# Performance work log

Hardware: AMD Instinct MI355X
Metric: run time of the kernel (lower is better)

Reference implementation:

```python
import jax, jax.numpy as jnp
import numpy as np

HF8_BIAS = 14  # exponent bias for the 1-4-3 hf8 layout; HF8_MAX = 2^(15-14)*1.875 = 3.75


def hf8_decode(bits):
    """Decode 8-bit hf8 codes (1 sign, 4 exp, 3 mantissa) to float.

    Mirrors convert.hf8_to_fp16: an elementwise dequant producing the
    fp16-valued weight tensor (computed here in fp32 for reference accuracy).
    """
    bits = bits.astype(jnp.int32)
    sign = jnp.where(((bits >> 7) & 1) == 1, -1.0, 1.0)
    exp = (bits >> 3) & 0xF
    man = (bits & 0x7).astype(jnp.float32)
    normal = jnp.exp2((exp - HF8_BIAS).astype(jnp.float32)) * (1.0 + man / 8.0)
    subnormal = jnp.exp2(jnp.float32(1 - HF8_BIAS)) * (man / 8.0)
    return sign * jnp.where(exp == 0, subnormal, normal)


def setup_inputs() -> dict:
    key = jax.random.key(0)
    k1, k2, k3 = jax.random.split(key, 3)
    B, Cin, Cout, H, W, K = 8, 320, 320, 64, 64, 3
    x = jax.random.normal(k1, (B, Cin, H, W), dtype=jnp.float32)
    w_bits = jax.random.randint(k2, (Cout, Cin, K, K), 0, 256, dtype=jnp.int32)
    b_bits = jax.random.randint(k3, (Cout,), 0, 256, dtype=jnp.int32)
    return {"x": x, "w_bits": w_bits, "b_bits": b_bits}


def reference(x, w_bits, b_bits):
    # dequant hf8 -> dense weight/bias (the fusible elementwise pass)
    w = hf8_decode(w_bits)          # [Cout, Cin, K, K]
    b = hf8_decode(b_bits)          # [Cout]
    # padding_mode == 'zeros' branch: plain conv2d, stride 1, pad 1, dilation 1, groups 1
    out = jax.lax.conv_general_dilated(
        x, w,
        window_strides=(1, 1),
        padding=((1, 1), (1, 1)),
        rhs_dilation=(1, 1),
        dimension_numbers=("NCHW", "OIHW", "NCHW"),
        feature_group_count=1,
    )
    return out + b[None, :, None, None]
```

## Files before the change

kernel.cpp:

```cpp
#include <hip/hip_runtime.h>
#include <stdint.h>

typedef short v8s __attribute__((ext_vector_type(8)));
typedef float v4f __attribute__((ext_vector_type(4)));
typedef unsigned int u32;

#define CIN   320
#define COUT  320
#define HH    64
#define WW    64
#define BN    80
#define NT    10
#define XSB   25344
#define WLB   15360
#define WKHB  61440

__device__ __forceinline__ float hf8_decode_f(int b) {
    int e = (b >> 3) & 15;
    int m = b & 7;
    float v = ldexpf((float)(e ? (8 + m) : m), e ? (e - 17) : -16);
    return ((b >> 7) & 1) ? -v : v;
}

__device__ __forceinline__ u32 cvt_pk_bf16(float lo, float hi) {
    u32 r;
    asm("v_cvt_pk_bf16_f32 %0, %1, %2" : "=v"(r) : "v"(lo), "v"(hi));
    return r;
}

__device__ __forceinline__ void gload16(const void* g, void* l) {
    __builtin_amdgcn_global_load_lds(
        (const __attribute__((address_space(1))) u32*)(uintptr_t)g,
        (__attribute__((address_space(3))) u32*)(uintptr_t)l, 16, 0, 0);
}

__global__ __launch_bounds__(256) void prepass_kernel(const int* __restrict__ w_bits,
                                                      const int* __restrict__ b_bits,
                                                      const float* __restrict__ x,
                                                      unsigned short* __restrict__ w_deq2,
                                                      float* __restrict__ b_deq,
                                                      unsigned short* __restrict__ x_t) {
    __shared__ __align__(16) unsigned short lt[32 * 64];
    const int tid = threadIdx.x;
    if (blockIdx.x < 3600) {
        int o  = blockIdx.x * 256 + tid;
        int e  = o & 7;
        int c2 = o >> 3;
        int co = c2 % COUT;
        int c3 = c2 / COUT;
        int cig = c3 & 3;
        int c4 = c3 >> 2;
        int kw = c4 % 3;
        int c5 = c4 / 3;
        int kh = c5 % 3;
        int t  = c5 / 3;
        int ci = t * 32 + cig * 8 + e;
        float v = hf8_decode_f(w_bits[(co * CIN + ci) * 9 + kh * 3 + kw] & 0xFF);
        w_deq2[o] = (unsigned short)(__float_as_uint(v) >> 16);
        if (o < COUT) b_deq[o] = hf8_decode_f(b_bits[o] & 0xFF);
        return;
    }
    const int b  = blockIdx.x - 3600;
    const int hp = b % 66;
    const int nc = b / 66;
    char* outp = (char*)x_t + (size_t)b * 4096;
    if (hp == 0 || hp == 65) {
        *(int4*)(outp + tid * 16) = make_int4(0, 0, 0, 0);
        return;
    }
    const int h = hp - 1;
    {
        int ci = tid >> 3, wg = tid & 7;
        const float* src = x + ((size_t)nc * 32 + ci) * (HH * WW) + h * WW + wg * 8;
        float4 a = *(const float4*)src;
        float4 c = *(const float4*)(src + 4);
        u32 d0 = cvt_pk_bf16(a.x, a.y);
        u32 d1 = cvt_pk_bf16(a.z, a.w);
        u32 d2 = cvt_pk_bf16(c.x, c.y);
        u32 d3 = cvt_pk_bf16(c.z, c.w);
        *(int4*)&lt[ci * 64 + wg * 8] = make_int4(d0, d1, d2, d3);
    }
    __syncthreads();
    if (tid < 128) {
        int w2 = tid & 31, o = tid >> 5;
        u32 A[4], B[4];
        #pragma unroll
        for (int j = 0; j < 4; ++j) {
            int p = o * 4 + j;
            u32 de = *(const u32*)&lt[(2 * p) * 64 + w2 * 2];
            u32 dq = *(const u32*)&lt[(2 * p + 1) * 64 + w2 * 2];
            A[j] = __builtin_amdgcn_perm(dq, de, 0x05040100u);
            B[j] = __builtin_amdgcn_perm(dq, de, 0x07060302u);
        }
        *(int4*)(outp + (2 * w2) * 64 + o * 16)     = make_int4(A[0], A[1], A[2], A[3]);
        *(int4*)(outp + (2 * w2 + 1) * 64 + o * 16) = make_int4(B[0], B[1], B[2], B[3]);
    }
}

__global__ __launch_bounds__(128, 1) void conv_phase_kernel(
        const unsigned short* __restrict__ x_t,
        const unsigned short* __restrict__ w_deq2,
        const float* __restrict__ b_deq,
        float* __restrict__ out) {
    __shared__ __align__(16) unsigned short xs[2 * XSB / 2];
    __shared__ __align__(16) unsigned short wl[2 * WLB / 2];

    const int tid  = threadIdx.x;
    const int bid  = blockIdx.x;
    const int cob  = bid >> 7;
    const int mb   = bid & 127;
    const int n    = mb >> 4;
    const int h0   = (mb & 15) << 2;
    const int wave = tid >> 6;
    const int lane = tid & 63;
    const int lhi  = lane >> 4;
    const int llo  = lane & 15;

    for (int i = tid; i < 384; i += 128) {
        int buf = i / 192;
        int r   = (i - buf * 192) >> 5;
        int rem = i & 31;
        int side = rem >> 4, e = rem & 15;
        *(u32*)((char*)xs + buf * XSB + r * 4224 + side * 4160 + e * 4) = 0;
    }

    int woffW[8];
    #pragma unroll
    for (int k = 0; k < 8; ++k) {
        int c = k * 128 + tid;
        int q = c / BN;
        int co = c - q * BN;
        woffW[k] = (q * COUT + cob * BN + co) << 4;
    }

    v4f acc[2][4][5];
    #pragma unroll
    for (int r = 0; r < 2; ++r)
        #pragma unroll
        for (int wc = 0; wc < 4; ++wc)
            #pragma unroll
            for (int j = 0; j < 5; ++j)
                acc[r][wc][j] = (v4f){0.f, 0.f, 0.f, 0.f};

    const char* xt_base = (const char*)x_t + ((size_t)(n * NT) * 66 + h0) * 4096;

    auto issueW = [&](int t_, int kh_, int wb) {
        const char* base = (const char*)w_deq2 + (size_t)(t_ * 3 + kh_) * WKHB;
        char* dst = (char*)wl + wb * WLB + tid * 16;
        #pragma unroll
        for (int k = 0; k < 8; ++k) {
            if (k * 128 + tid < 960)
                gload16(base + woffW[k], dst + k * 2048);
        }
    };
    auto issueX = [&](int t_, int xb) {
        const char* src = xt_base + (size_t)t_ * (66 * 4096);
        char* dstb = (char*)xs + xb * XSB;
        #pragma unroll
        for (int k = 0; k < 12; ++k) {
            int c = k * 128 + tid;
            int j = c >> 8;
            int u = c & 255;
            gload16(src + j * 4096 + u * 16, dstb + j * 4224 + 64 + u * 16);
        }
    };
    auto computeKh = [&](int kh, int xb, int wb) {
        const char* xp = (const char*)xs + xb * XSB + (2 * wave + kh) * 4224;
        const unsigned short* wp = wl + wb * (WLB / 2);
        __builtin_amdgcn_s_setprio(1);
        #pragma unroll
        for (int kw = 0; kw < 3; ++kw) {
            v8s bfr[5];
            #pragma unroll
            for (int nr = 0; nr < 5; ++nr)
                bfr[nr] = *(const v8s*)&wp[((kw * 4 + lhi) * BN + nr * 16 + llo) * 8];
            #pragma unroll
            for (int r = 0; r < 2; ++r)
                #pragma unroll
                for (int wc = 0; wc < 4; ++wc) {
                    v8s afr = *(const v8s*)(xp + r * 4224 + (wc * 16 + llo + kw) * 64 + lhi * 16);
                    #pragma unroll
                    for (int nr = 0; nr < 5; ++nr)
                        acc[r][wc][nr] = __builtin_amdgcn_mfma_f32_16x16x32_bf16(
                            afr, bfr[nr], acc[r][wc][nr], 0, 0, 0);
                }
        }
        __builtin_amdgcn_s_setprio(0);
    };

    issueW(0, 0, 0);
    issueX(0, 0);

    for (int t = 0; t < NT; ++t) {
        const int p = t & 1;
        __syncthreads();
        issueW(t, 1, p ^ 1);
        computeKh(0, p, p);
        __syncthreads();
        issueW(t, 2, p);
        computeKh(1, p, p ^ 1);
        __syncthreads();
        if (t + 1 < NT) { issueW(t + 1, 0, p ^ 1); issueX(t + 1, p ^ 1); }
        computeKh(2, p, p);
    }

    #pragma unroll
    for (int nr = 0; nr < 5; ++nr) {
        int co = cob * BN + nr * 16 + llo;
        float bias = b_deq[co];
        #pragma unroll
        for (int r = 0; r < 2; ++r) {
            int h = h0 + 2 * wave + r;
            float* op = out + ((size_t)(n * COUT + co) * HH + h) * WW + lhi * 4;
            #pragma unroll
            for (int wc = 0; wc < 4; ++wc) {
                float4 o;
                o.x = acc[r][wc][nr][0] + bias;
                o.y = acc[r][wc][nr][1] + bias;
                o.z = acc[r][wc][nr][2] + bias;
                o.w = acc[r][wc][nr][3] + bias;
                *(float4*)(op + wc * 16) = o;
            }
        }
    }
}

extern "C" void kernel_launch(void* const* d_in, const int* in_sizes, int n_in,
                              void* d_out, int out_size, void* d_ws, size_t ws_size,
                              hipStream_t stream) {
    const float* x      = (const float*)d_in[0];
    const int*   w_bits = (const int*)d_in[1];
    const int*   b_bits = (const int*)d_in[2];
    float*       out    = (float*)d_out;

    unsigned short* w_deq2 = (unsigned short*)d_ws;
    float*          b_deq  = (float*)((char*)d_ws + 1843200);
    unsigned short* x_t    = (unsigned short*)((char*)d_ws + (2u << 20));

    prepass_kernel<<<8880, 256, 0, stream>>>(w_bits, b_bits, x, w_deq2, b_deq, x_t);
    conv_phase_kernel<<<512, 128, 0, stream>>>(x_t, w_deq2, b_deq, out);
}
```

Baseline: 74.19 us.

## Restructure conv into 4-wave blocks with per-tap triple-buffered weight pipeline

The conv kernel moves from 2 waves with 2 output rows each to 4 waves with one row each, and asks for 2 blocks per CU. Weights are now streamed one (kh,kw) tap at a time into a triple-buffered LDS ring. Loads are issued two taps ahead, with explicit vmcnt waits and one barrier per tap instead of full-kh double buffering. The aim is to raise occupancy, shrink LDS per block, and overlap global-to-LDS loads with MFMA work more finely, at the cost of more barriers and hand-tuned waitcnt counts that must match the number of outstanding loads.

```diff
diff --git a/kernel.cpp b/kernel.cpp
--- a/kernel.cpp
+++ b/kernel.cpp
@@ -5,15 +5,15 @@
 typedef float v4f __attribute__((ext_vector_type(4)));
 typedef unsigned int u32;
 
-#define CIN   320
-#define COUT  320
-#define HH    64
-#define WW    64
-#define BN    80
-#define NT    10
-#define XSB   25344
-#define WLB   15360
-#define WKHB  61440
+#define CIN    320
+#define COUT   320
+#define HH     64
+#define WW     64
+#define BN     80
+#define NT     10
+#define XSB    25344
+#define WLBUF  5120
+#define WSLICE 20480
 
 __device__ __forceinline__ float hf8_decode_f(int b) {
     int e = (b >> 3) & 15;
@@ -37,7 +37,7 @@
 __global__ __launch_bounds__(256) void prepass_kernel(const int* __restrict__ w_bits,
                                                       const int* __restrict__ b_bits,
                                                       const float* __restrict__ x,
-                                                      unsigned short* __restrict__ w_deq2,
+                                                      unsigned short* __restrict__ w_deq3,
                                                       float* __restrict__ b_deq,
                                                       unsigned short* __restrict__ x_t) {
     __shared__ __align__(16) unsigned short lt[32 * 64];
@@ -49,14 +49,13 @@
         int co = c2 % COUT;
         int c3 = c2 / COUT;
         int cig = c3 & 3;
-        int c4 = c3 >> 2;
-        int kw = c4 % 3;
-        int c5 = c4 / 3;
-        int kh = c5 % 3;
-        int t  = c5 / 3;
+        int g  = c3 >> 2;
+        int kw = g % 3;
+        int kh = (g / 3) % 3;
+        int t  = g / 9;
         int ci = t * 32 + cig * 8 + e;
         float v = hf8_decode_f(w_bits[(co * CIN + ci) * 9 + kh * 3 + kw] & 0xFF);
-        w_deq2[o] = (unsigned short)(__float_as_uint(v) >> 16);
+        w_deq3[o] = (unsigned short)(__float_as_uint(v) >> 16);
         if (o < COUT) b_deq[o] = hf8_decode_f(b_bits[o] & 0xFF);
         return;
     }
@@ -97,13 +96,13 @@
     }
 }
 
-__global__ __launch_bounds__(128, 1) void conv_phase_kernel(
+__global__ __launch_bounds__(256, 2) void conv_t4_kernel(
         const unsigned short* __restrict__ x_t,
-        const unsigned short* __restrict__ w_deq2,
+        const unsigned short* __restrict__ w_deq3,
         const float* __restrict__ b_deq,
         float* __restrict__ out) {
     __shared__ __align__(16) unsigned short xs[2 * XSB / 2];
-    __shared__ __align__(16) unsigned short wl[2 * WLB / 2];
+    __shared__ __align__(16) unsigned short wl[3 * WLBUF / 2];
 
     const int tid  = threadIdx.x;
     const int bid  = blockIdx.x;
@@ -116,7 +115,7 @@
     const int lhi  = lane >> 4;
     const int llo  = lane & 15;
 
-    for (int i = tid; i < 384; i += 128) {
+    for (int i = tid; i < 384; i += 256) {
         int buf = i / 192;
         int r   = (i - buf * 192) >> 5;
         int rem = i & 31;
@@ -124,103 +123,105 @@
         *(u32*)((char*)xs + buf * XSB + r * 4224 + side * 4160 + e * 4) = 0;
     }
 
-    int woffW[8];
-    #pragma unroll
-    for (int k = 0; k < 8; ++k) {
-        int c = k * 128 + tid;
-        int q = c / BN;
-        int co = c - q * BN;
-        woffW[k] = (q * COUT + cob * BN + co) << 4;
-    }
-
-    v4f acc[2][4][5];
-    #pragma unroll
-    for (int r = 0; r < 2; ++r)
-        #pragma unroll
-        for (int wc = 0; wc < 4; ++wc)
-            #pragma unroll
-            for (int j = 0; j < 5; ++j)
-                acc[r][wc][j] = (v4f){0.f, 0.f, 0.f, 0.f};
-
-    const char* xt_base = (const char*)x_t + ((size_t)(n * NT) * 66 + h0) * 4096;
-
-    auto issueW = [&](int t_, int kh_, int wb) {
-        const char* base = (const char*)w_deq2 + (size_t)(t_ * 3 + kh_) * WKHB;
-        char* dst = (char*)wl + wb * WLB + tid * 16;
-        #pragma unroll
-        for (int k = 0; k < 8; ++k) {
-            if (k * 128 + tid < 960)
-                gload16(base + woffW[k], dst + k * 2048);
-        }
+    int woffW[2], wdst[2];
+    #pragma unroll
+    for (int k = 0; k < 2; ++k) {
+        int jj  = wave * 2 + k;
+        int cmb = (jj * 64) % 320;
+        int cm  = cmb + lane;
+        int cig = cm / BN;
+        int co  = cm - cig * BN;
+        woffW[k] = (cig * COUT + cob * BN + co) << 4;
+        wdst[k]  = cmb << 4;
+    }
+
+    v4f acc[4][5];
+    #pragma unroll
+    for (int i = 0; i < 4; ++i)
+        #pragma unroll
+        for (int j = 0; j < 5; ++j)
+            acc[i][j] = (v4f){0.f, 0.f, 0.f, 0.f};
+
+    const char* xt_lane = (const char*)x_t + ((size_t)(n * NT) * 66 + h0) * 4096 + lane * 16;
+
+    auto issueW = [&](int g, int buf) {
+        const char* base = (const char*)w_deq3 + (size_t)g * WSLICE;
+        char* dst = (char*)wl + buf * WLBUF;
+        gload16(base + woffW[0], dst + wdst[0]);
+        gload16(base + woffW[1], dst + wdst[1]);
     };
-    auto issueX = [&](int t_, int xb) {
-        const char* src = xt_base + (size_t)t_ * (66 * 4096);
-        char* dstb = (char*)xs + xb * XSB;
-        #pragma unroll
-        for (int k = 0; k < 12; ++k) {
-            int c = k * 128 + tid;
-            int j = c >> 8;
-            int u = c & 255;
-            gload16(src + j * 4096 + u * 16, dstb + j * 4224 + 64 + u * 16);
-        }
+    auto issueX1 = [&](int tt, int xb, int m) {
+        int id = wave * 6 + m;
+        int j = id >> 2, k = id & 3;
+        gload16(xt_lane + (size_t)tt * (66 * 4096) + j * 4096 + k * 1024,
+                (char*)xs + xb * XSB + j * 4224 + 64 + k * 1024);
     };
-    auto computeKh = [&](int kh, int xb, int wb) {
-        const char* xp = (const char*)xs + xb * XSB + (2 * wave + kh) * 4224;
-        const unsigned short* wp = wl + wb * (WLB / 2);
+    auto phaseCompute = [&](int kh, int kw, int xb, int buf) {
+        const unsigned short* wp = (const unsigned short*)((const char*)wl + buf * WLBUF);
+        const char* xp = (const char*)xs + xb * XSB + (wave + kh) * 4224;
+        v8s bfr[5];
+        #pragma unroll
+        for (int nr = 0; nr < 5; ++nr)
+            bfr[nr] = *(const v8s*)&wp[(lhi * BN + nr * 16 + llo) * 8];
         __builtin_amdgcn_s_setprio(1);
         #pragma unroll
-        for (int kw = 0; kw < 3; ++kw) {
-            v8s bfr[5];
+        for (int mr = 0; mr < 4; ++mr) {
+            v8s afr = *(const v8s*)(xp + (mr * 16 + llo + kw) * 64 + lhi * 16);
             #pragma unroll
             for (int nr = 0; nr < 5; ++nr)
-                bfr[nr] = *(const v8s*)&wp[((kw * 4 + lhi) * BN + nr * 16 + llo) * 8];
-            #pragma unroll
-            for (int r = 0; r < 2; ++r)
-                #pragma unroll
-                for (int wc = 0; wc < 4; ++wc) {
-                    v8s afr = *(const v8s*)(xp + r * 4224 + (wc * 16 + llo + kw) * 64 + lhi * 16);
-                    #pragma unroll
-                    for (int nr = 0; nr < 5; ++nr)
-                        acc[r][wc][nr] = __builtin_amdgcn_mfma_f32_16x16x32_bf16(
-                            afr, bfr[nr], acc[r][wc][nr], 0, 0, 0);
-                }
+                acc[mr][nr] = __builtin_amdgcn_mfma_f32_16x16x32_bf16(
+                    afr, bfr[nr], acc[mr][nr], 0, 0, 0);
         }
         __builtin_amdgcn_s_setprio(0);
     };
 
-    issueW(0, 0, 0);
-    issueX(0, 0);
+    issueW(0, 0);
+    #pragma unroll
+    for (int m = 0; m < 6; ++m) issueX1(0, 0, m);
+    issueW(1, 1);
+    asm volatile("s_waitcnt lgkmcnt(0)" ::: "memory");
+
+#define PHASE(I, NSTR)                                                        \
+    {                                                                         \
+        if (t == NT - 1) { asm volatile("s_waitcnt vmcnt(0)" ::: "memory"); } \
+        else             { asm volatile("s_waitcnt vmcnt(" NSTR ")" ::: "memory"); } \
+        __builtin_amdgcn_s_barrier();                                         \
+        __builtin_amdgcn_sched_barrier(0);                                    \
+        int g2 = t * 9 + (I) + 2;                                             \
+        if (g2 <= 89) issueW(g2, ((I) + 2) % 3);                              \
+        if ((I) <= 5 && t + 1 < NT) issueX1(t + 1, p ^ 1, (I));               \
+        phaseCompute((I) / 3, (I) % 3, p, (I) % 3);                           \
+    }
 
     for (int t = 0; t < NT; ++t) {
         const int p = t & 1;
-        __syncthreads();
-        issueW(t, 1, p ^ 1);
-        computeKh(0, p, p);
-        __syncthreads();
-        issueW(t, 2, p);
-        computeKh(1, p, p ^ 1);
-        __syncthreads();
-        if (t + 1 < NT) { issueW(t + 1, 0, p ^ 1); issueX(t + 1, p ^ 1); }
-        computeKh(2, p, p);
-    }
-
+        PHASE(0, "2")
+        PHASE(1, "3")
+        PHASE(2, "4")
+        PHASE(3, "4")
+        PHASE(4, "4")
+        PHASE(5, "4")
+        PHASE(6, "4")
+        PHASE(7, "3")
+        PHASE(8, "2")
+    }
+#undef PHASE
+
+    const int h = h0 + wave;
     #pragma unroll
     for (int nr = 0; nr < 5; ++nr) {
         int co = cob * BN + nr * 16 + llo;
         float bias = b_deq[co];
-        #pragma unroll
-        for (int r = 0; r < 2; ++r) {
-            int h = h0 + 2 * wave + r;
-            float* op = out + ((size_t)(n * COUT + co) * HH + h) * WW + lhi * 4;
-            #pragma unroll
-            for (int wc = 0; wc < 4; ++wc) {
-                float4 o;
-                o.x = acc[r][wc][nr][0] + bias;
-                o.y = acc[r][wc][nr][1] + bias;
-                o.z = acc[r][wc][nr][2] + bias;
-                o.w = acc[r][wc][nr][3] + bias;
-                *(float4*)(op + wc * 16) = o;
-            }
+        float* op = out + ((size_t)(n * COUT + co) * HH + h) * WW;
+        #pragma unroll
+        for (int mr = 0; mr < 4; ++mr) {
+            int wc = mr * 16 + lhi * 4;
+            float4 o;
+            o.x = acc[mr][nr][0] + bias;
+            o.y = acc[mr][nr][1] + bias;
+            o.z = acc[mr][nr][2] + bias;
+            o.w = acc[mr][nr][3] + bias;
+            *(float4*)(op + wc) = o;
         }
     }
 }
@@ -233,10 +234,10 @@
     const int*   b_bits = (const int*)d_in[2];
     float*       out    = (float*)d_out;
 
-    unsigned short* w_deq2 = (unsigned short*)d_ws;
+    unsigned short* w_deq3 = (unsigned short*)d_ws;
     float*          b_deq  = (float*)((char*)d_ws + 1843200);
     unsigned short* x_t    = (unsigned short*)((char*)d_ws + (2u << 20));
 
-    prepass_kernel<<<8880, 256, 0, stream>>>(w_bits, b_bits, x, w_deq2, b_deq, x_t);
-    conv_phase_kernel<<<512, 128, 0, stream>>>(x_t, w_deq2, b_deq, out);
-}
+    prepass_kernel<<<8880, 256, 0, stream>>>(w_bits, b_bits, x, w_deq3, b_deq, x_t);
+    conv_t4_kernel<<<512, 256, 0, stream>>>(x_t, w_deq3, b_deq, out);
+}
```

Measured after the change: 68.53 us. 1.08x faster.
